# Performance work log

Measured on AMD Instinct MI355X. Metric: run time of the kernel, lower is better.

The kernel has to match this reference:

```python
import jax, jax.numpy as jnp
import numpy as np

D_MODEL = 1024
H = 16
D_HEAD = D_MODEL // H  # 64
RANK = 32
ALPHA = 1.0


def _lora_linear(x, W, b, dW, dB):
    # merged weight: W + alpha * (dB @ dW), then x @ W_merged.T + b
    Wm = W + ALPHA * (dB @ dW)
    return x @ Wm.T + b


def setup_inputs() -> dict:
    key = jax.random.key(0)
    ks = jax.random.split(key, 20)
    inp = {"x": jax.random.normal(ks[0], (2, 2048, D_MODEL), dtype=jnp.float32)}
    i = 1
    for name in ("q", "k", "v", "o"):
        inp[f"{name}_W"] = jax.random.normal(ks[i], (D_MODEL, D_MODEL), dtype=jnp.float32) * 0.02; i += 1
        inp[f"{name}_b"] = jnp.zeros((D_MODEL,), dtype=jnp.float32)
        inp[f"{name}_dW"] = jax.random.normal(ks[i], (RANK, D_MODEL), dtype=jnp.float32) * 0.01; i += 1
        inp[f"{name}_dB"] = jax.random.normal(ks[i], (D_MODEL, RANK), dtype=jnp.float32) * 0.01; i += 1
    return inp


def reference(x, q_W, q_b, q_dW, q_dB, k_W, k_b, k_dW, k_dB,
              v_W, v_b, v_dW, v_dB, o_W, o_b, o_dW, o_dB):
    b_s, n, _ = x.shape
    # LoRA-merged QKV projections
    q = _lora_linear(x, q_W, q_b, q_dW, q_dB).reshape(b_s, n, H, D_HEAD)
    k = _lora_linear(x, k_W, k_b, k_dW, k_dB).reshape(b_s, n, H, D_HEAD)
    v = _lora_linear(x, v_W, v_b, v_dW, v_dB).reshape(b_s, n, H, D_HEAD)
    scale = 1.0 / np.sqrt(D_HEAD).astype(np.float32)
    # att: [b, h, nq, nk]
    att = jnp.einsum('bqhd,bkhd->bhqk', q, k) * scale
    att = jax.nn.softmax(att, axis=-1)  # dropout = identity (eval mode)
    out = jnp.einsum('bhqk,bkhd->bqhd', att, v).reshape(b_s, n, H * D_HEAD)
    return _lora_linear(out, o_W, o_b, o_dW, o_dB)
```

## Files before the change

kernel.cpp:

```cpp
#include <hip/hip_runtime.h>

typedef unsigned short ushort_t;
typedef unsigned int u32;
typedef __attribute__((ext_vector_type(8))) short short8;
typedef __attribute__((ext_vector_type(4))) float floatx4;

typedef const __attribute__((address_space(1))) u32* gptr_t;
typedef __attribute__((address_space(3))) u32* lptr_t;

__device__ __forceinline__ void async_copy16(void* lds, const void* g) {
  __builtin_amdgcn_global_load_lds((gptr_t)g, (lptr_t)lds, 16, 0, 0);
}

__device__ __forceinline__ ushort_t f2bf(float f) {
  u32 u = __float_as_uint(f);
  u += 0x7fffu + ((u >> 16) & 1u);
  return (ushort_t)(u >> 16);
}

__device__ __forceinline__ floatx4 mfma16(short8 a, short8 b, floatx4 c) {
  return __builtin_amdgcn_mfma_f32_16x16x32_bf16(a, b, c, 0, 0, 0);
}

struct alignas(16) F4 { float a, b, c, d; };
struct alignas(8) U4 { ushort_t a, b, c, d; };

#define QSCALE 0.18033688011112043f

__global__ __launch_bounds__(256) void prep_kernel(
    const float* __restrict__ x, ushort_t* __restrict__ xs,
    const float* __restrict__ W0, const float* __restrict__ dW0, const float* __restrict__ dB0,
    const float* __restrict__ W1, const float* __restrict__ dW1, const float* __restrict__ dB1,
    const float* __restrict__ W2, const float* __restrict__ dW2, const float* __restrict__ dB2,
    const float* __restrict__ W3, const float* __restrict__ dW3, const float* __restrict__ dB3,
    ushort_t* __restrict__ Wm) {
  const int bid = blockIdx.x;
  if (bid < 4096) {
    int i = bid * 256 + threadIdx.x;
    F4 v = ((const F4*)x)[i];
    U4 hh = {f2bf(v.a), f2bf(v.b), f2bf(v.c), f2bf(v.d)};
    ((U4*)xs)[i] = hh;
    return;
  }
  const int t = bid - 4096;
  const int layer = t >> 7, sub = t & 127;
  const float* W = (layer == 0) ? W0 : (layer == 1) ? W1 : (layer == 2) ? W2 : W3;
  const float* dW = (layer == 0) ? dW0 : (layer == 1) ? dW1 : (layer == 2) ? dW2 : dW3;
  const float* dB = (layer == 0) ? dB0 : (layer == 1) ? dB1 : (layer == 2) ? dB2 : dB3;
  ushort_t* Wh = Wm + (size_t)layer * 1024 * 1024;
  const int ot = sub * 8;
  const int d0 = threadIdx.x * 4;
  float acc[8][4] = {};
  for (int r = 0; r < 32; ++r) {
    F4 w = *(const F4*)&dW[r * 1024 + d0];
    float wv[4] = {w.a, w.b, w.c, w.d};
#pragma unroll
    for (int o = 0; o < 8; ++o) {
      float s = dB[(ot + o) * 32 + r];
#pragma unroll
      for (int j = 0; j < 4; ++j) acc[o][j] += s * wv[j];
    }
  }
#pragma unroll
  for (int o = 0; o < 8; ++o) {
    F4 w = *(const F4*)&W[(ot + o) * 1024 + d0];
    U4 hh = {f2bf(w.a + acc[o][0]), f2bf(w.b + acc[o][1]),
             f2bf(w.c + acc[o][2]), f2bf(w.d + acc[o][3])};
    *(U4*)&Wh[(ot + o) * 1024 + d0] = hh;
  }
}

template <int MODE, int TN>
__global__ __launch_bounds__(256) void gemm_bt(
    const ushort_t* __restrict__ A, const ushort_t* __restrict__ B,
    const float* __restrict__ b0, const float* __restrict__ b1,
    const float* __restrict__ b2,
    ushort_t* __restrict__ C, ushort_t* __restrict__ vth,
    float* __restrict__ Cf, const int M, const int N, const int K) {
  constexpr int NT2 = TN / 32;
  __shared__ __align__(16) ushort_t lA[128 * 32], lB[TN * 32];
  const int tid = threadIdx.x;
  const int wave = tid >> 6, lane = tid & 63;
  const int lo4 = lane & 15, quad = lane >> 4;
  const int n0 = blockIdx.x * TN, m0 = blockIdx.y * 128;
  const int wm = (wave >> 1) * 64, wn = (wave & 1) * (TN / 2);

  floatx4 acc[4][NT2];
  const floatx4 zero4 = {0.f, 0.f, 0.f, 0.f};
#pragma unroll
  for (int mt = 0; mt < 4; ++mt)
#pragma unroll
    for (int nt = 0; nt < NT2; ++nt) acc[mt][nt] = zero4;

  const int strow = lane >> 2;
  const int stcol = (lane & 3) * 8;

  for (int kk = 0; kk < K; kk += 32) {
#pragma unroll
    for (int i = 0; i < 2; ++i) {
      const int g = wave * 2 + i;
      async_copy16(&lA[g * 512], A + (size_t)(m0 + g * 16 + strow) * K + kk + stcol);
    }
#pragma unroll
    for (int i = 0; i < TN / 64; ++i) {
      const int g = wave * (TN / 64) + i;
      async_copy16(&lB[g * 512], B + (size_t)(n0 + g * 16 + strow) * K + kk + stcol);
    }
    __syncthreads();
    short8 a_[4], b_[NT2];
#pragma unroll
    for (int t = 0; t < 4; ++t)
      a_[t] = *(const short8*)&lA[(wm + t * 16 + lo4) * 32 + quad * 8];
#pragma unroll
    for (int t = 0; t < NT2; ++t)
      b_[t] = *(const short8*)&lB[(wn + t * 16 + lo4) * 32 + quad * 8];
#pragma unroll
    for (int mt = 0; mt < 4; ++mt)
#pragma unroll
      for (int nt = 0; nt < NT2; ++nt) acc[mt][nt] = mfma16(a_[mt], b_[nt], acc[mt][nt]);
    __syncthreads();
  }

#pragma unroll
  for (int nt = 0; nt < NT2; ++nt) {
    const int col = n0 + wn + nt * 16 + lo4;
    float bias;
    if (MODE == 0)
      bias = (col < 1024) ? b0[col] : (col < 2048) ? b1[col - 1024] : b2[col - 2048];
    else
      bias = b0[col];
#pragma unroll
    for (int mt = 0; mt < 4; ++mt)
#pragma unroll
      for (int r = 0; r < 4; ++r) {
        const int row = m0 + wm + mt * 16 + quad * 4 + r;
        float c = acc[mt][nt][r] + bias;
        if (MODE == 0) {
          if (col < 1024) c *= QSCALE;
          ushort_t hv = f2bf(c);
          if (col < 2048) {
            C[(size_t)row * 2048 + col] = hv;
          } else {
            const int d = col - 2048;
            const size_t vrow = (size_t)(((row >> 11) * 16 + (d >> 6)) * 64 + (d & 63));
            vth[vrow * 2048 + (row & 2047)] = hv;
          }
        } else {
          Cf[(size_t)row * N + col] = c;
        }
      }
  }
}

__global__ __launch_bounds__(512) void attn_kernel(
    const ushort_t* __restrict__ qk, const ushort_t* __restrict__ vt,
    ushort_t* __restrict__ at) {
  __shared__ __align__(16) ushort_t Kh[2][64 * 64], Vh[2][64 * 64];
  __shared__ __align__(16) ushort_t P[8][16][72];
  const int qt = blockIdx.x, bh = blockIdx.y;
  const int b = bh >> 4, h = bh & 15;
  const int tid = threadIdx.x;
  const int wave = tid >> 6, lane = tid & 63;
  const int half = wave >> 2, w4 = wave & 3;
  const int lo4 = lane & 15, quad = lane >> 4;

  short8 qh[2];
  {
    const size_t g = (size_t)(b * 2048 + qt * 64 + w4 * 16 + lo4) * 2048 + h * 64 + quad * 8;
    qh[0] = *(const short8*)(qk + g);
    qh[1] = *(const short8*)(qk + g + 32);
  }
  float l_acc[4] = {0.f, 0.f, 0.f, 0.f};
  const floatx4 zero4 = {0.f, 0.f, 0.f, 0.f};
  floatx4 O[4];
#pragma unroll
  for (int nt = 0; nt < 4; ++nt) O[nt] = zero4;

  const int strow = lane >> 3;
  const int stcol = ((lane & 7) ^ strow) * 8;

  for (int it = 0; it < 16; ++it) {
    const int kt = half * 16 + it;
#pragma unroll
    for (int i = 0; i < 2; ++i) {
      const int row = w4 * 16 + i * 8 + strow;
      const int uoff = (w4 * 16 + i * 8) * 64;
      const size_t kg = (size_t)(b * 2048 + kt * 64 + row) * 2048 + 1024 + h * 64 + stcol;
      async_copy16(&Kh[half][uoff], qk + kg);
      const size_t vg = (size_t)(bh * 64 + row) * 2048 + kt * 64 + stcol;
      async_copy16(&Vh[half][uoff], vt + vg);
    }
    __syncthreads();

    floatx4 s[4];
#pragma unroll
    for (int nt = 0; nt < 4; ++nt) s[nt] = zero4;
#pragma unroll
    for (int nt = 0; nt < 4; ++nt)
#pragma unroll
      for (int ks = 0; ks < 2; ++ks) {
        const int off = (nt * 16 + lo4) * 64 + (((ks * 4 + quad) ^ (lo4 & 7)) * 8);
        s[nt] = mfma16(qh[ks], *(const short8*)&Kh[half][off], s[nt]);
      }

#pragma unroll
    for (int nt = 0; nt < 4; ++nt)
#pragma unroll
      for (int r = 0; r < 4; ++r) {
        float pv = __builtin_amdgcn_exp2f(s[nt][r]);
        s[nt][r] = pv;
        P[wave][quad * 4 + r][nt * 16 + lo4] = (ushort_t)(__float_as_uint(pv) >> 16);
      }
#pragma unroll
    for (int r = 0; r < 4; ++r)
      l_acc[r] += (s[0][r] + s[1][r]) + (s[2][r] + s[3][r]);

#pragma unroll
    for (int ks = 0; ks < 2; ++ks) {
      short8 pf = *(const short8*)&P[wave][lo4][ks * 32 + quad * 8];
#pragma unroll
      for (int nt = 0; nt < 4; ++nt) {
        const int off = (nt * 16 + lo4) * 64 + (((ks * 4 + quad) ^ (lo4 & 7)) * 8);
        O[nt] = mfma16(pf, *(const short8*)&Vh[half][off], O[nt]);
      }
    }
    __syncthreads();
  }

#pragma unroll
  for (int r = 0; r < 4; ++r) {
    float s = l_acc[r];
    s += __shfl_xor(s, 1);
    s += __shfl_xor(s, 2);
    s += __shfl_xor(s, 4);
    s += __shfl_xor(s, 8);
    l_acc[r] = s;
  }

  float* Om = (float*)&Kh[0][0];
  float* Lm = (float*)&Vh[0][0];
  if (half == 1) {
#pragma unroll
    for (int nt = 0; nt < 4; ++nt)
#pragma unroll
      for (int r = 0; r < 4; ++r)
        Om[(w4 * 16 + quad * 4 + r) * 64 + nt * 16 + lo4] = O[nt][r];
    if (lo4 == 0) {
#pragma unroll
      for (int r = 0; r < 4; ++r) Lm[w4 * 16 + quad * 4 + r] = l_acc[r];
    }
  }
  __syncthreads();
  if (half == 0) {
    float linv[4];
#pragma unroll
    for (int r = 0; r < 4; ++r)
      linv[r] = 1.f / (l_acc[r] + Lm[w4 * 16 + quad * 4 + r]);
#pragma unroll
    for (int nt = 0; nt < 4; ++nt)
#pragma unroll
      for (int r = 0; r < 4; ++r) {
        float o = (O[nt][r] + Om[(w4 * 16 + quad * 4 + r) * 64 + nt * 16 + lo4]) * linv[r];
        const size_t row = (size_t)(b * 2048 + qt * 64 + w4 * 16 + quad * 4 + r);
        at[row * 1024 + h * 64 + nt * 16 + lo4] = f2bf(o);
      }
  }
}

extern "C" void kernel_launch(void* const* d_in, const int* in_sizes, int n_in,
                              void* d_out, int out_size, void* d_ws, size_t ws_size,
                              hipStream_t stream) {
  const float* x = (const float*)d_in[0];
  const float* qW = (const float*)d_in[1];
  const float* qb = (const float*)d_in[2];
  const float* qdW = (const float*)d_in[3];
  const float* qdB = (const float*)d_in[4];
  const float* kW = (const float*)d_in[5];
  const float* kb = (const float*)d_in[6];
  const float* kdW = (const float*)d_in[7];
  const float* kdB = (const float*)d_in[8];
  const float* vW = (const float*)d_in[9];
  const float* vb = (const float*)d_in[10];
  const float* vdW = (const float*)d_in[11];
  const float* vdB = (const float*)d_in[12];
  const float* oW = (const float*)d_in[13];
  const float* ob = (const float*)d_in[14];
  const float* odW = (const float*)d_in[15];
  const float* odB = (const float*)d_in[16];

  char* ws = (char*)d_ws;
  const size_t MB = 1024u * 1024u;
  const size_t WELEM = 1024u * 1024u;
  ushort_t* xs = (ushort_t*)(ws + 0 * MB);
  ushort_t* Wm = (ushort_t*)(ws + 8 * MB);
  ushort_t* qk = (ushort_t*)(ws + 16 * MB);
  ushort_t* vt = (ushort_t*)(ws + 32 * MB);
  ushort_t* at = xs;

  prep_kernel<<<4608, 256, 0, stream>>>(x, xs, qW, qdW, qdB, kW, kdW, kdB,
                                        vW, vdW, vdB, oW, odW, odB, Wm);
  gemm_bt<0, 128><<<dim3(24, 32), 256, 0, stream>>>(xs, Wm, qb, kb, vb,
                                                    qk, vt, nullptr, 4096, 3072, 1024);
  attn_kernel<<<dim3(32, 32), 512, 0, stream>>>(qk, vt, at);
  gemm_bt<1, 64><<<dim3(16, 32), 256, 0, stream>>>(at, Wm + 3 * WELEM, ob, nullptr,
                                                   nullptr, nullptr, nullptr,
                                                   (float*)d_out, 4096, 1024, 1024);
}
```

Before: 247.0 us.

## Double-buffer GEMM and attention LDS tiles; restructure attention to 128-query blocks

Both the GEMM and the attention kernel now double-buffer their LDS tiles. The next K tile is prefetched asynchronously while MFMAs run on the current one, and one barrier per iteration is removed. The attention kernel drops its split-KV scheme, where two half-blocks each covered 16 key tiles and were merged through LDS. Instead all 8 waves take distinct query rows, 128 queries per block, and sweep all 32 key tiles, which halves the grid and removes the merge step. In exchange there are fewer blocks for occupancy, and the LDS usage of the GEMM doubles.

```diff
diff --git a/kernel.cpp b/kernel.cpp
--- a/kernel.cpp
+++ b/kernel.cpp
@@ -78,7 +78,7 @@
     ushort_t* __restrict__ C, ushort_t* __restrict__ vth,
     float* __restrict__ Cf, const int M, const int N, const int K) {
   constexpr int NT2 = TN / 32;
-  __shared__ __align__(16) ushort_t lA[128 * 32], lB[TN * 32];
+  __shared__ __align__(16) ushort_t lA[2][128 * 32], lB[2][TN * 32];
   const int tid = threadIdx.x;
   const int wave = tid >> 6, lane = tid & 63;
   const int lo4 = lane & 15, quad = lane >> 4;
@@ -95,30 +95,48 @@
   const int strow = lane >> 2;
   const int stcol = (lane & 3) * 8;
 
-  for (int kk = 0; kk < K; kk += 32) {
+  const int NTILES = K >> 5;
+  {
 #pragma unroll
     for (int i = 0; i < 2; ++i) {
       const int g = wave * 2 + i;
-      async_copy16(&lA[g * 512], A + (size_t)(m0 + g * 16 + strow) * K + kk + stcol);
+      async_copy16(&lA[0][g * 512], A + (size_t)(m0 + g * 16 + strow) * K + stcol);
     }
 #pragma unroll
     for (int i = 0; i < TN / 64; ++i) {
       const int g = wave * (TN / 64) + i;
-      async_copy16(&lB[g * 512], B + (size_t)(n0 + g * 16 + strow) * K + kk + stcol);
-    }
-    __syncthreads();
+      async_copy16(&lB[0][g * 512], B + (size_t)(n0 + g * 16 + strow) * K + stcol);
+    }
+  }
+  __syncthreads();
+
+  for (int t = 0; t < NTILES; ++t) {
+    const int cur = t & 1;
+    if (t + 1 < NTILES) {
+      const int kk = (t + 1) << 5;
+#pragma unroll
+      for (int i = 0; i < 2; ++i) {
+        const int g = wave * 2 + i;
+        async_copy16(&lA[cur ^ 1][g * 512], A + (size_t)(m0 + g * 16 + strow) * K + kk + stcol);
+      }
+#pragma unroll
+      for (int i = 0; i < TN / 64; ++i) {
+        const int g = wave * (TN / 64) + i;
+        async_copy16(&lB[cur ^ 1][g * 512], B + (size_t)(n0 + g * 16 + strow) * K + kk + stcol);
+      }
+    }
     short8 a_[4], b_[NT2];
 #pragma unroll
-    for (int t = 0; t < 4; ++t)
-      a_[t] = *(const short8*)&lA[(wm + t * 16 + lo4) * 32 + quad * 8];
-#pragma unroll
-    for (int t = 0; t < NT2; ++t)
-      b_[t] = *(const short8*)&lB[(wn + t * 16 + lo4) * 32 + quad * 8];
+    for (int t2 = 0; t2 < 4; ++t2)
+      a_[t2] = *(const short8*)&lA[cur][(wm + t2 * 16 + lo4) * 32 + quad * 8];
+#pragma unroll
+    for (int t2 = 0; t2 < NT2; ++t2)
+      b_[t2] = *(const short8*)&lB[cur][(wn + t2 * 16 + lo4) * 32 + quad * 8];
 #pragma unroll
     for (int mt = 0; mt < 4; ++mt)
 #pragma unroll
       for (int nt = 0; nt < NT2; ++nt) acc[mt][nt] = mfma16(a_[mt], b_[nt], acc[mt][nt]);
-    __syncthreads();
+    if (t + 1 < NTILES) __syncthreads();
   }
 
 #pragma unroll
@@ -161,12 +179,11 @@
   const int b = bh >> 4, h = bh & 15;
   const int tid = threadIdx.x;
   const int wave = tid >> 6, lane = tid & 63;
-  const int half = wave >> 2, w4 = wave & 3;
   const int lo4 = lane & 15, quad = lane >> 4;
 
   short8 qh[2];
   {
-    const size_t g = (size_t)(b * 2048 + qt * 64 + w4 * 16 + lo4) * 2048 + h * 64 + quad * 8;
+    const size_t g = (size_t)(b * 2048 + qt * 128 + wave * 16 + lo4) * 2048 + h * 64 + quad * 8;
     qh[0] = *(const short8*)(qk + g);
     qh[1] = *(const short8*)(qk + g + 32);
   }
@@ -178,19 +195,21 @@
 
   const int strow = lane >> 3;
   const int stcol = ((lane & 7) ^ strow) * 8;
-
-  for (int it = 0; it < 16; ++it) {
-    const int kt = half * 16 + it;
-#pragma unroll
-    for (int i = 0; i < 2; ++i) {
-      const int row = w4 * 16 + i * 8 + strow;
-      const int uoff = (w4 * 16 + i * 8) * 64;
-      const size_t kg = (size_t)(b * 2048 + kt * 64 + row) * 2048 + 1024 + h * 64 + stcol;
-      async_copy16(&Kh[half][uoff], qk + kg);
-      const size_t vg = (size_t)(bh * 64 + row) * 2048 + kt * 64 + stcol;
-      async_copy16(&Vh[half][uoff], vt + vg);
-    }
-    __syncthreads();
+  const int srow = wave * 8 + strow;
+  const int uoff = wave * 8 * 64;
+
+  async_copy16(&Kh[0][uoff], qk + (size_t)(b * 2048 + srow) * 2048 + 1024 + h * 64 + stcol);
+  async_copy16(&Vh[0][uoff], vt + (size_t)(bh * 64 + srow) * 2048 + stcol);
+  __syncthreads();
+
+  for (int kt = 0; kt < 32; ++kt) {
+    const int cur = kt & 1;
+    if (kt + 1 < 32) {
+      const int kn = (kt + 1) * 64;
+      async_copy16(&Kh[cur ^ 1][uoff],
+                   qk + (size_t)(b * 2048 + kn + srow) * 2048 + 1024 + h * 64 + stcol);
+      async_copy16(&Vh[cur ^ 1][uoff], vt + (size_t)(bh * 64 + srow) * 2048 + kn + stcol);
+    }
 
     floatx4 s[4];
 #pragma unroll
@@ -200,7 +219,7 @@
 #pragma unroll
       for (int ks = 0; ks < 2; ++ks) {
         const int off = (nt * 16 + lo4) * 64 + (((ks * 4 + quad) ^ (lo4 & 7)) * 8);
-        s[nt] = mfma16(qh[ks], *(const short8*)&Kh[half][off], s[nt]);
+        s[nt] = mfma16(qh[ks], *(const short8*)&Kh[cur][off], s[nt]);
       }
 
 #pragma unroll
@@ -221,12 +240,13 @@
 #pragma unroll
       for (int nt = 0; nt < 4; ++nt) {
         const int off = (nt * 16 + lo4) * 64 + (((ks * 4 + quad) ^ (lo4 & 7)) * 8);
-        O[nt] = mfma16(pf, *(const short8*)&Vh[half][off], O[nt]);
-      }
-    }
-    __syncthreads();
-  }
-
+        O[nt] = mfma16(pf, *(const short8*)&Vh[cur][off], O[nt]);
+      }
+    }
+    if (kt + 1 < 32) __syncthreads();
+  }
+
+  float linv[4];
 #pragma unroll
   for (int r = 0; r < 4; ++r) {
     float s = l_acc[r];
@@ -234,37 +254,16 @@
     s += __shfl_xor(s, 2);
     s += __shfl_xor(s, 4);
     s += __shfl_xor(s, 8);
-    l_acc[r] = s;
-  }
-
-  float* Om = (float*)&Kh[0][0];
-  float* Lm = (float*)&Vh[0][0];
-  if (half == 1) {
-#pragma unroll
-    for (int nt = 0; nt < 4; ++nt)
-#pragma unroll
-      for (int r = 0; r < 4; ++r)
-        Om[(w4 * 16 + quad * 4 + r) * 64 + nt * 16 + lo4] = O[nt][r];
-    if (lo4 == 0) {
-#pragma unroll
-      for (int r = 0; r < 4; ++r) Lm[w4 * 16 + quad * 4 + r] = l_acc[r];
-    }
-  }
-  __syncthreads();
-  if (half == 0) {
-    float linv[4];
-#pragma unroll
-    for (int r = 0; r < 4; ++r)
-      linv[r] = 1.f / (l_acc[r] + Lm[w4 * 16 + quad * 4 + r]);
-#pragma unroll
-    for (int nt = 0; nt < 4; ++nt)
-#pragma unroll
-      for (int r = 0; r < 4; ++r) {
-        float o = (O[nt][r] + Om[(w4 * 16 + quad * 4 + r) * 64 + nt * 16 + lo4]) * linv[r];
-        const size_t row = (size_t)(b * 2048 + qt * 64 + w4 * 16 + quad * 4 + r);
-        at[row * 1024 + h * 64 + nt * 16 + lo4] = f2bf(o);
-      }
-  }
+    linv[r] = 1.f / s;
+  }
+#pragma unroll
+  for (int nt = 0; nt < 4; ++nt)
+#pragma unroll
+    for (int r = 0; r < 4; ++r) {
+      float o = O[nt][r] * linv[r];
+      const size_t row = (size_t)(b * 2048 + qt * 128 + wave * 16 + quad * 4 + r);
+      at[row * 1024 + h * 64 + nt * 16 + lo4] = f2bf(o);
+    }
 }
 
 extern "C" void kernel_launch(void* const* d_in, const int* in_sizes, int n_in,
@@ -301,7 +300,7 @@
                                         vW, vdW, vdB, oW, odW, odB, Wm);
   gemm_bt<0, 128><<<dim3(24, 32), 256, 0, stream>>>(xs, Wm, qb, kb, vb,
                                                     qk, vt, nullptr, 4096, 3072, 1024);
-  attn_kernel<<<dim3(32, 32), 512, 0, stream>>>(qk, vt, at);
+  attn_kernel<<<dim3(16, 32), 512, 0, stream>>>(qk, vt, at);
   gemm_bt<1, 64><<<dim3(16, 32), 256, 0, stream>>>(at, Wm + 3 * WELEM, ob, nullptr,
                                                    nullptr, nullptr, nullptr,
                                                    (float*)d_out, 4096, 1024, 1024);
```

Result: faster. 232.8 us (-5.8%).
